# Performance work log

Measured on AMD Instinct MI355X. Metric: run time of the kernel, lower is better.

The kernel has to match this reference:

```python
import jax, jax.numpy as jnp
import numpy as np

CLIP_LEN = 8      # == num_frame
NUM_NODES = 7     # == group_size
NUM_BASIC = 1024
NUM_MIXED = 8192
T = 2 * CLIP_LEN - 1          # 15 temporal offsets
N = 1 + NUM_NODES * CLIP_LEN  # 57 graph size


def setup_inputs() -> dict:
    key = jax.random.key(0)
    k1, k2, k3, k4 = jax.random.split(key, 4)
    mat = jax.random.normal(k1, (NUM_BASIC, NUM_NODES, NUM_NODES), dtype=jnp.float32)
    temp_extent = jax.random.normal(k2, (NUM_BASIC, T), dtype=jnp.float32)
    # nn.Linear(num_basic, num_mixed): weight [out,in], bias [out]
    W = jax.random.normal(k3, (NUM_MIXED, NUM_BASIC), dtype=jnp.float32) * (1.0 / np.sqrt(NUM_BASIC))
    b = jax.random.normal(k4, (NUM_MIXED,), dtype=jnp.float32) * 0.01
    return {"mat": mat, "temp_extent": temp_extent, "W": W, "b": b}


def reference(mat, temp_extent, W, b):
    n, cl = NUM_NODES, CLIP_LEN
    Hb = mat.shape[0]
    te = jax.nn.sigmoid(temp_extent) + 1.0                      # [Hb, T]
    x = jnp.einsum('ht,hnm->htmn', te, mat)                     # [Hb, T, n, n]
    x = jax.nn.relu(x)
    x = jnp.transpose(x, (1, 2, 3, 0)).reshape(T * n, n, Hb)    # (t m) n h
    y = x @ W.T + b                                             # [(t m), n, Hm]
    y = jax.nn.relu(jnp.transpose(y, (2, 1, 0)))                # [Hm, n, T*n]
    Hm = y.shape[0]
    # vectorized version of the per-frame slice-write loop:
    # frame i reads cols n*(cl-1-i) : n*(2*cl-1-i) of y
    starts = n * (cl - 1 - jnp.arange(cl))                      # [cl]
    idx = starts[:, None] + jnp.arange(n * cl)[None, :]         # [cl, n*cl]
    blocks = y[:, :, idx]                                       # [Hm, n, cl, n*cl]
    blocks = jnp.transpose(blocks, (0, 2, 1, 3)).reshape(Hm, n * cl, n * cl)
    base = jnp.zeros((Hm, N, N), dtype=y.dtype)
    base = base.at[:, 0::7, 0::7].set(1.0)                      # person-node anchors
    mixed = base.at[:, 1:, 1:].set(blocks)                      # [Hm, N, N]
    # degree normalization D^{-1/2} A D^{-1/2} (row sums, clamped at 1)
    d = jnp.clip(mixed.sum(axis=2), 1.0, None) ** -0.5          # [Hm, N]
    ret = d[:, :, None] * mixed * d[:, None, :]
    return ret
```

## Files before the change

kernel.cpp:

```cpp
#include <hip/hip_runtime.h>
#include <hip/hip_bf16.h>

#define HB 1024
#define HM 8192
#define NR 735
#define NPAD 768
#define NOUT 57

typedef __attribute__((ext_vector_type(8))) _Float16 half8;
typedef __attribute__((ext_vector_type(4))) _Float16 half4v;
typedef __attribute__((ext_vector_type(4))) float floatx4;

__global__ __launch_bounds__(256) void prep_x2_kernel(
    const float* __restrict__ mat, const float* __restrict__ tex,
    _Float16* __restrict__ Xh) {
  const int r = blockIdx.x;
  const int n = r % 7;
  const int tm = r / 7;
  const int m = tm % 7;
  const int t = tm / 7;
#pragma unroll
  for (int i = 0; i < 4; ++i) {
    const int h = i * 256 + threadIdx.x;
    float v = 0.f;
    if (r < NR) {
      const float mv = mat[h * 49 + n * 7 + m];
      const float te = 1.f / (1.f + expf(-tex[h * 15 + t])) + 1.f;
      v = te * mv;
      v = v > 0.f ? v : 0.f;
    }
    Xh[r * HB + h] = (_Float16)v;
  }
}

__global__ __launch_bounds__(256) void prep_w_kernel(
    const float4* __restrict__ W, half4v* __restrict__ Wh) {
  const int idx = blockIdx.x * 256 + threadIdx.x;
  const float4 v = W[idx];
  half4v h;
  h.x = (_Float16)v.x;
  h.y = (_Float16)v.y;
  h.z = (_Float16)v.z;
  h.w = (_Float16)v.w;
  Wh[idx] = h;
}

__global__ __launch_bounds__(256) void gemm_kernel(
    const _Float16* __restrict__ A,
    const _Float16* __restrict__ B,
    const float* __restrict__ bias,
    float* __restrict__ Y) {
  __shared__ __align__(16) _Float16 As[128 * 32];
  __shared__ __align__(16) _Float16 Bs[128 * 32];

  const int tid = threadIdx.x;
  const int lane = tid & 63;
  const int wave = tid >> 6;
  const int bm = blockIdx.x;
  const int bn = blockIdx.y;
  const int wm = (wave >> 1) * 64;
  const int wn = (wave & 1) * 64;

  floatx4 acc[4][4] = {};

  const int srow = lane >> 2;
  const int skh = (lane & 3) * 8;
  const size_t abase = (size_t)(bm * 128) * HB;
  const size_t bbase = (size_t)(bn * 128) * HB;

  const int mrow = lane & 15;
  const int quad = lane >> 4;

  for (int k0 = 0; k0 < HB; k0 += 32) {
#pragma unroll
    for (int it = 0; it < 2; ++it) {
      const int chunk = wave * 2 + it;
      const int row = chunk * 16 + srow;
      __builtin_amdgcn_global_load_lds(
          (const __attribute__((address_space(1))) void*)(A + abase + (size_t)row * HB + k0 + skh),
          (__attribute__((address_space(3))) void*)(As + chunk * 512), 16, 0, 0);
      __builtin_amdgcn_global_load_lds(
          (const __attribute__((address_space(1))) void*)(B + bbase + (size_t)row * HB + k0 + skh),
          (__attribute__((address_space(3))) void*)(Bs + chunk * 512), 16, 0, 0);
    }
    __syncthreads();

    half8 af[4], bf[4];
#pragma unroll
    for (int i = 0; i < 4; ++i) {
      af[i] = *(const half8*)(As + (wm + i * 16 + mrow) * 32 + quad * 8);
      bf[i] = *(const half8*)(Bs + (wn + i * 16 + mrow) * 32 + quad * 8);
    }
#pragma unroll
    for (int i = 0; i < 4; ++i)
#pragma unroll
      for (int j = 0; j < 4; ++j)
        acc[i][j] = __builtin_amdgcn_mfma_f32_16x16x32_f16(af[i], bf[j], acc[i][j], 0, 0, 0);
    __syncthreads();
  }

#pragma unroll
  for (int i = 0; i < 4; ++i) {
#pragma unroll
    for (int j = 0; j < 4; ++j) {
#pragma unroll
      for (int reg = 0; reg < 4; ++reg) {
        const int grow = bm * 128 + wm + i * 16 + quad * 4 + reg;
        const int gcol = bn * 128 + wn + j * 16 + mrow;
        float v = acc[i][j][reg] + bias[grow];
        v = v > 0.f ? v : 0.f;
        Y[(size_t)grow * NPAD + gcol] = v;
      }
    }
  }
}

__global__ __launch_bounds__(256) void epilogue_kernel(
    const float* __restrict__ Y, float* __restrict__ out) {
  const int j = blockIdx.x;
  __shared__ float ly[NR];
  __shared__ float dd[NOUT];

  const float* yj = Y + (size_t)j * NPAD;
  for (int i = threadIdx.x; i < NR; i += 256) ly[i] = yj[i];
  __syncthreads();

  if (threadIdx.x < NOUT) {
    const int r = threadIdx.x;
    float s;
    if (r == 0) {
      s = 9.f;
    } else {
      const int c = (r - 1) / 7;
      const int n = (r - 1) % 7;
      const int base = 7 * (7 - c);
      s = (n == 6) ? 1.f : 0.f;
#pragma unroll
      for (int p = 0; p < 56; ++p) s += ly[(base + p) * 7 + n];
    }
    s = s < 1.f ? 1.f : s;
    dd[r] = rsqrtf(s);
  }
  __syncthreads();

  float* oj = out + (size_t)j * (NOUT * NOUT);
  for (int i = threadIdx.x; i < NOUT * NOUT; i += 256) {
    const int r = i / NOUT;
    const int q = i % NOUT;
    float v;
    if (r == 0) {
      v = (q % 7 == 0) ? dd[0] * dd[q] : 0.f;
    } else {
      const int c = (r - 1) / 7;
      const int n = (r - 1) % 7;
      if (q == 0)
        v = (n == 6) ? dd[r] * dd[0] : 0.f;
      else
        v = dd[r] * ly[(7 * (7 - c) + q - 1) * 7 + n] * dd[q];
    }
    oj[i] = v;
  }
}

extern "C" void kernel_launch(void* const* d_in, const int* in_sizes, int n_in,
                              void* d_out, int out_size, void* d_ws, size_t ws_size,
                              hipStream_t stream) {
  const float* mat = (const float*)d_in[0];
  const float* tex = (const float*)d_in[1];
  const float* W = (const float*)d_in[2];
  const float* b = (const float*)d_in[3];
  float* out = (float*)d_out;

  char* ws = (char*)d_ws;
  _Float16* Xh = (_Float16*)(ws);
  _Float16* Wh = (_Float16*)(ws + (size_t)NPAD * HB * 2);
  float* Y = (float*)(ws + (size_t)NPAD * HB * 2 + (size_t)HM * HB * 2);

  prep_x2_kernel<<<NPAD, 256, 0, stream>>>(mat, tex, Xh);
  prep_w_kernel<<<HM * HB / 4 / 256, 256, 0, stream>>>((const float4*)W, (half4v*)Wh);
  gemm_kernel<<<dim3(HM / 128, NPAD / 128), 256, 0, stream>>>(Wh, Xh, b, Y);
  epilogue_kernel<<<HM, 256, 0, stream>>>(Y, out);
}
```

Before: 185.6 us.

## Merge prep kernels, double-buffer GEMM with smaller tiles, parallelize degree sums

Fuses the X and W fp16 conversion kernels into one launch. The GEMM now uses 64x128 tiles, which doubles the block count for occupancy. It double-buffers LDS so the next K-slice loads while the current one feeds the MFMAs, and remaps block IDs so each group of 8 consecutive blocks works on different A-tiles. The epilogue splits each row-sum across 4 lanes and combines them with shuffles. The smaller tiles mean less data reuse per block, and the prefetch relies on a single barrier per iteration being enough to keep the two buffers apart.

```diff
diff --git a/kernel.cpp b/kernel.cpp
--- a/kernel.cpp
+++ b/kernel.cpp
@@ -1,5 +1,4 @@
 #include <hip/hip_runtime.h>
-#include <hip/hip_bf16.h>
 
 #define HB 1024
 #define HM 8192
@@ -7,106 +6,132 @@
 #define NPAD 768
 #define NOUT 57
 
+#define BM 64
+#define BN 128
+#define BK 32
+
 typedef __attribute__((ext_vector_type(8))) _Float16 half8;
 typedef __attribute__((ext_vector_type(4))) _Float16 half4v;
 typedef __attribute__((ext_vector_type(4))) float floatx4;
 
-__global__ __launch_bounds__(256) void prep_x2_kernel(
+__global__ __launch_bounds__(256) void prep_kernel(
     const float* __restrict__ mat, const float* __restrict__ tex,
-    _Float16* __restrict__ Xh) {
-  const int r = blockIdx.x;
-  const int n = r % 7;
-  const int tm = r / 7;
-  const int m = tm % 7;
-  const int t = tm / 7;
-#pragma unroll
-  for (int i = 0; i < 4; ++i) {
-    const int h = i * 256 + threadIdx.x;
-    float v = 0.f;
-    if (r < NR) {
-      const float mv = mat[h * 49 + n * 7 + m];
-      const float te = 1.f / (1.f + expf(-tex[h * 15 + t])) + 1.f;
-      v = te * mv;
-      v = v > 0.f ? v : 0.f;
-    }
-    Xh[r * HB + h] = (_Float16)v;
-  }
-}
-
-__global__ __launch_bounds__(256) void prep_w_kernel(
-    const float4* __restrict__ W, half4v* __restrict__ Wh) {
-  const int idx = blockIdx.x * 256 + threadIdx.x;
-  const float4 v = W[idx];
-  half4v h;
-  h.x = (_Float16)v.x;
-  h.y = (_Float16)v.y;
-  h.z = (_Float16)v.z;
-  h.w = (_Float16)v.w;
-  Wh[idx] = h;
-}
+    const float4* __restrict__ W,
+    _Float16* __restrict__ Xh, half4v* __restrict__ Wh) {
+  const int blk = blockIdx.x;
+  if (blk < NPAD) {
+    const int r = blk;
+    const int n = r % 7;
+    const int tm = r / 7;
+    const int m = tm % 7;
+    const int t = tm / 7;
+#pragma unroll
+    for (int i = 0; i < 4; ++i) {
+      const int h = i * 256 + threadIdx.x;
+      float v = 0.f;
+      if (r < NR) {
+        const float mv = mat[h * 49 + n * 7 + m];
+        const float te = 1.f / (1.f + expf(-tex[h * 15 + t])) + 1.f;
+        v = te * mv;
+        v = v > 0.f ? v : 0.f;
+      }
+      Xh[r * HB + h] = (_Float16)v;
+    }
+  } else {
+    const int idx = (blk - NPAD) * 256 + threadIdx.x;
+    const float4 v = W[idx];
+    half4v h;
+    h.x = (_Float16)v.x;
+    h.y = (_Float16)v.y;
+    h.z = (_Float16)v.z;
+    h.w = (_Float16)v.w;
+    Wh[idx] = h;
+  }
+}
+
+#define STAGE(p, k0)                                                           \
+  do {                                                                         \
+    const int arow_ = wave * 16 + srow;                                        \
+    __builtin_amdgcn_global_load_lds(                                          \
+        (const __attribute__((address_space(1))) void*)(                       \
+            A + abase + (size_t)arow_ * HB + (k0) + skh),                      \
+        (__attribute__((address_space(3))) void*)(&As[p][wave * 512]),         \
+        16, 0, 0);                                                             \
+    _Pragma("unroll")                                                          \
+    for (int it_ = 0; it_ < 2; ++it_) {                                        \
+      const int chunk_ = wave * 2 + it_;                                       \
+      const int brow_ = chunk_ * 16 + srow;                                    \
+      __builtin_amdgcn_global_load_lds(                                        \
+          (const __attribute__((address_space(1))) void*)(                     \
+              B + bbase + (size_t)brow_ * HB + (k0) + skh),                    \
+          (__attribute__((address_space(3))) void*)(&Bs[p][chunk_ * 512]),     \
+          16, 0, 0);                                                           \
+    }                                                                          \
+  } while (0)
 
 __global__ __launch_bounds__(256) void gemm_kernel(
     const _Float16* __restrict__ A,
     const _Float16* __restrict__ B,
     const float* __restrict__ bias,
     float* __restrict__ Y) {
-  __shared__ __align__(16) _Float16 As[128 * 32];
-  __shared__ __align__(16) _Float16 Bs[128 * 32];
+  __shared__ __align__(16) _Float16 As[2][BM * BK];
+  __shared__ __align__(16) _Float16 Bs[2][BN * BK];
 
   const int tid = threadIdx.x;
   const int lane = tid & 63;
   const int wave = tid >> 6;
-  const int bm = blockIdx.x;
-  const int bn = blockIdx.y;
-  const int wm = (wave >> 1) * 64;
+
+  const int bid = blockIdx.x;
+  const int wg = (bid & 7) * 96 + (bid >> 3);
+  const int bn = wg % 6;
+  const int bm = wg / 6;
+
+  const int wm = (wave >> 1) * 32;
   const int wn = (wave & 1) * 64;
 
-  floatx4 acc[4][4] = {};
+  floatx4 acc[2][4] = {};
 
   const int srow = lane >> 2;
   const int skh = (lane & 3) * 8;
-  const size_t abase = (size_t)(bm * 128) * HB;
-  const size_t bbase = (size_t)(bn * 128) * HB;
+  const size_t abase = (size_t)(bm * BM) * HB;
+  const size_t bbase = (size_t)(bn * BN) * HB;
 
   const int mrow = lane & 15;
   const int quad = lane >> 4;
 
-  for (int k0 = 0; k0 < HB; k0 += 32) {
-#pragma unroll
-    for (int it = 0; it < 2; ++it) {
-      const int chunk = wave * 2 + it;
-      const int row = chunk * 16 + srow;
-      __builtin_amdgcn_global_load_lds(
-          (const __attribute__((address_space(1))) void*)(A + abase + (size_t)row * HB + k0 + skh),
-          (__attribute__((address_space(3))) void*)(As + chunk * 512), 16, 0, 0);
-      __builtin_amdgcn_global_load_lds(
-          (const __attribute__((address_space(1))) void*)(B + bbase + (size_t)row * HB + k0 + skh),
-          (__attribute__((address_space(3))) void*)(Bs + chunk * 512), 16, 0, 0);
-    }
+  STAGE(0, 0);
+  __syncthreads();
+
+  int p = 0;
+  for (int k0 = 0; k0 < HB; k0 += BK) {
+    if (k0 + BK < HB) STAGE(p ^ 1, k0 + BK);
+
+    half8 af[2], bf[4];
+#pragma unroll
+    for (int i = 0; i < 2; ++i)
+      af[i] = *(const half8*)(&As[p][(wm + i * 16 + mrow) * BK + quad * 8]);
+#pragma unroll
+    for (int j = 0; j < 4; ++j)
+      bf[j] = *(const half8*)(&Bs[p][(wn + j * 16 + mrow) * BK + quad * 8]);
+#pragma unroll
+    for (int i = 0; i < 2; ++i)
+#pragma unroll
+      for (int j = 0; j < 4; ++j)
+        acc[i][j] =
+            __builtin_amdgcn_mfma_f32_16x16x32_f16(af[i], bf[j], acc[i][j], 0, 0, 0);
+
     __syncthreads();
-
-    half8 af[4], bf[4];
-#pragma unroll
-    for (int i = 0; i < 4; ++i) {
-      af[i] = *(const half8*)(As + (wm + i * 16 + mrow) * 32 + quad * 8);
-      bf[i] = *(const half8*)(Bs + (wn + i * 16 + mrow) * 32 + quad * 8);
-    }
-#pragma unroll
-    for (int i = 0; i < 4; ++i)
-#pragma unroll
-      for (int j = 0; j < 4; ++j)
-        acc[i][j] = __builtin_amdgcn_mfma_f32_16x16x32_f16(af[i], bf[j], acc[i][j], 0, 0, 0);
-    __syncthreads();
-  }
-
-#pragma unroll
-  for (int i = 0; i < 4; ++i) {
+    p ^= 1;
+  }
+
+#pragma unroll
+  for (int i = 0; i < 2; ++i) {
 #pragma unroll
     for (int j = 0; j < 4; ++j) {
 #pragma unroll
       for (int reg = 0; reg < 4; ++reg) {
-        const int grow = bm * 128 + wm + i * 16 + quad * 4 + reg;
-        const int gcol = bn * 128 + wn + j * 16 + mrow;
+        const int grow = bm * BM + wm + i * 16 + quad * 4 + reg;
+        const int gcol = bn * BN + wn + j * 16 + mrow;
         float v = acc[i][j][reg] + bias[grow];
         v = v > 0.f ? v : 0.f;
         Y[(size_t)grow * NPAD + gcol] = v;
@@ -125,21 +150,26 @@
   for (int i = threadIdx.x; i < NR; i += 256) ly[i] = yj[i];
   __syncthreads();
 
-  if (threadIdx.x < NOUT) {
-    const int r = threadIdx.x;
-    float s;
+  if (threadIdx.x < 4 * NOUT) {
+    const int r = threadIdx.x >> 2;
+    const int sub = threadIdx.x & 3;
+    float s = 0.f;
     if (r == 0) {
-      s = 9.f;
+      s = (sub == 0) ? 9.f : 0.f;
     } else {
       const int c = (r - 1) / 7;
       const int n = (r - 1) % 7;
       const int base = 7 * (7 - c);
-      s = (n == 6) ? 1.f : 0.f;
-#pragma unroll
-      for (int p = 0; p < 56; ++p) s += ly[(base + p) * 7 + n];
-    }
-    s = s < 1.f ? 1.f : s;
-    dd[r] = rsqrtf(s);
+      if (sub == 0) s = (n == 6) ? 1.f : 0.f;
+#pragma unroll
+      for (int p = sub; p < 56; p += 4) s += ly[(base + p) * 7 + n];
+    }
+    s += __shfl_xor(s, 1);
+    s += __shfl_xor(s, 2);
+    if (sub == 0) {
+      s = s < 1.f ? 1.f : s;
+      dd[r] = rsqrtf(s);
+    }
   }
   __syncthreads();
 
@@ -176,8 +206,8 @@
   _Float16* Wh = (_Float16*)(ws + (size_t)NPAD * HB * 2);
   float* Y = (float*)(ws + (size_t)NPAD * HB * 2 + (size_t)HM * HB * 2);
 
-  prep_x2_kernel<<<NPAD, 256, 0, stream>>>(mat, tex, Xh);
-  prep_w_kernel<<<HM * HB / 4 / 256, 256, 0, stream>>>((const float4*)W, (half4v*)Wh);
-  gemm_kernel<<<dim3(HM / 128, NPAD / 128), 256, 0, stream>>>(Wh, Xh, b, Y);
+  prep_kernel<<<NPAD + HM * HB / 4 / 256, 256, 0, stream>>>(
+      mat, tex, (const float4*)W, Xh, (half4v*)Wh);
+  gemm_kernel<<<HM / BM * (NPAD / BN), 256, 0, stream>>>(Wh, Xh, b, Y);
   epilogue_kernel<<<HM, 256, 0, stream>>>(Y, out);
 }
```

Measured after the change: 185.1 us. No clear change (-0.3%).
